# Kernel optimization log

Hardware: AMD Instinct MI355X
Metric: run time of the kernel (lower is better)

Reference implementation:

```python
import jax, jax.numpy as jnp
import numpy as np

N_SRC, N_MID, N_TGT = 200000, 100000, 50000
E1, E2 = 1600000, 800000
D_IN, D_HID, D_OUT = 128, 256, 64


def setup_inputs() -> dict:
    key = jax.random.key(0)
    ks = jax.random.split(key, 10)
    x = jax.random.normal(ks[0], (N_SRC, D_IN), dtype=jnp.float32)
    # edge_index[0] = source node ids, edge_index[1] = target node ids (PyG source_to_target)
    ei1 = jnp.stack([
        jax.random.randint(ks[1], (E1,), 0, N_SRC, dtype=jnp.int32),
        jax.random.randint(ks[2], (E1,), 0, N_MID, dtype=jnp.int32),
    ])
    ei2 = jnp.stack([
        jax.random.randint(ks[3], (E2,), 0, N_MID, dtype=jnp.int32),
        jax.random.randint(ks[4], (E2,), 0, N_TGT, dtype=jnp.int32),
    ])
    s = 1.0 / np.sqrt(D_IN)
    Wl1 = jax.random.uniform(ks[5], (D_IN, D_HID), jnp.float32, -s, s)
    Wr1 = jax.random.uniform(ks[6], (D_IN, D_HID), jnp.float32, -s, s)
    b1 = jnp.zeros((D_HID,), jnp.float32)
    s2 = 1.0 / np.sqrt(D_HID)
    Wl2 = jax.random.uniform(ks[7], (D_HID, D_OUT), jnp.float32, -s2, s2)
    Wr2 = jax.random.uniform(ks[8], (D_HID, D_OUT), jnp.float32, -s2, s2)
    b2 = jnp.zeros((D_OUT,), jnp.float32)
    return {"x": x, "edge_index1": ei1, "edge_index2": ei2,
            "Wl1": Wl1, "Wr1": Wr1, "b1": b1,
            "Wl2": Wl2, "Wr2": Wr2, "b2": b2}


def _sage_conv(x_src, x_tgt, edge_index, Wl, Wr, b, n_tgt):
    # mean aggregation of source features onto targets, then two linear branches
    msg = x_src[edge_index[0]]                                   # [E, d]
    agg = jax.ops.segment_sum(msg, edge_index[1], num_segments=n_tgt)
    cnt = jax.ops.segment_sum(jnp.ones((edge_index.shape[1],), x_src.dtype),
                              edge_index[1], num_segments=n_tgt)
    agg = agg / jnp.maximum(cnt, 1.0)[:, None]
    return agg @ Wl + x_tgt @ Wr + b


def reference(x, edge_index1, edge_index2, Wl1, Wr1, b1, Wl2, Wr2, b2):
    # layer 1: [N_SRC, D_IN] -> [N_MID, D_HID], then ReLU (dropout inactive in eval)
    h = _sage_conv(x, x[:N_MID], edge_index1, Wl1, Wr1, b1, N_MID)
    h = jax.nn.relu(h)
    # layer 2 (final): no activation
    out = _sage_conv(h, h[:N_TGT], edge_index2, Wl2, Wr2, b2, N_TGT)
    return out
```

## Files before the change

### kernel.cpp

```cpp
#include <hip/hip_runtime.h>


#define NSRC 200000
#define NMID 100000
#define NTGT 50000
#define NE1  1600000
#define NE2  800000
#define DIN  128
#define DHID 256
#define DOUT 64

#define XCH (NSRC * 16)

#define CH   4096
#define NBK1 391
#define NBK2 196
#define NCH1 ((NE1 + CH - 1) / CH)
#define NCH2 ((NE2 + CH - 1) / CH)
#define HCH  8192
#define NHC1 ((NE1 + HCH - 1) / HCH)
#define NHC2 ((NE2 + HCH - 1) / HCH)
#define NHIST (NHC1 + NHC2)
#define CVB ((XCH + 65536 + 32768 + 255) / 256)
#define MAXBUF 6144

typedef __attribute__((ext_vector_type(8))) short bf16x8;
typedef __attribute__((ext_vector_type(4))) float f32x4;
typedef __attribute__((ext_vector_type(2))) float f32x2;

__device__ __forceinline__ unsigned short f2bf(float f) {
    unsigned int u = __builtin_bit_cast(unsigned int, f);
    u += 0x7FFFu + ((u >> 16) & 1u);
    return (unsigned short)(u >> 16);
}
__device__ __forceinline__ float bf_lo(unsigned int u) {
    return __builtin_bit_cast(float, u << 16);
}
__device__ __forceinline__ float bf_hi(unsigned int u) {
    return __builtin_bit_cast(float, u & 0xFFFF0000u);
}
__device__ __forceinline__ float bf1(unsigned short u) {
    return __builtin_bit_cast(float, (unsigned int)u << 16);
}

__global__ __launch_bounds__(256) void conv_hist_kernel(
    const float* __restrict__ x,
    const float* __restrict__ Wl1, const float* __restrict__ Wr1,
    const float* __restrict__ Wl2, const float* __restrict__ Wr2,
    unsigned short* __restrict__ xb, unsigned short* __restrict__ WT1,
    unsigned short* __restrict__ WT2,
    const int* __restrict__ ei1, const int* __restrict__ ei2,
    int* __restrict__ bhist1, int* __restrict__ bhist2)
{
    __shared__ unsigned int lh[512];
    if (blockIdx.x < NHIST) {
        const int* ei; int* bh; int nE, nbk, chunk;
        if (blockIdx.x < NHC1) { ei = ei1; bh = bhist1; nE = NE1; nbk = NBK1; chunk = blockIdx.x; }
        else { ei = ei2; bh = bhist2; nE = NE2; nbk = NBK2; chunk = blockIdx.x - NHC1; }
        int t = threadIdx.x;
        lh[t] = 0; lh[t + 256] = 0;
        __syncthreads();
        int base = chunk * HCH;
        int end = nE < base + HCH ? nE : base + HCH;
        for (int e = base + t; e < end; e += 256)
            atomicAdd(&lh[((unsigned)ei[nE + e]) >> 8], 1u);
        __syncthreads();
        if (t < nbk && lh[t]) atomicAdd(&bh[t], (int)lh[t]);
        if (t + 256 < nbk && lh[t + 256]) atomicAdd(&bh[t + 256], (int)lh[t + 256]);
        return;
    }
    int gid = (blockIdx.x - NHIST) * 256 + threadIdx.x;
    if (gid < XCH) {
        const float4 v0 = *(const float4*)(x + (long long)gid * 8);
        const float4 v1 = *(const float4*)(x + (long long)gid * 8 + 4);
        unsigned short o[8] = {f2bf(v0.x), f2bf(v0.y), f2bf(v0.z), f2bf(v0.w),
                               f2bf(v1.x), f2bf(v1.y), f2bf(v1.z), f2bf(v1.w)};
        *(uint4*)(xb + (long long)gid * 8) = *(const uint4*)o;
        return;
    }
    int g = gid - XCH;
    if (g < 65536) {
        int n = g >> 8, k = g & 255;
        float v = (k < DIN) ? Wl1[(long long)k * DHID + n]
                            : Wr1[(long long)(k - DIN) * DHID + n];
        WT1[g] = f2bf(v);
        return;
    }
    g -= 65536;
    if (g < 32768) {
        int n2 = g >> 8, k = g & 255;
        float v = (n2 < DOUT) ? Wl2[(long long)k * DOUT + n2]
                              : Wr2[(long long)k * DOUT + (n2 - DOUT)];
        WT2[g] = f2bf(v);
    }
}


__global__ __launch_bounds__(256) void bucket_scan_kernel(
    const int* __restrict__ bhist1, const int* __restrict__ bhist2,
    int* __restrict__ bbase1, int* __restrict__ bbase2,
    int* __restrict__ bcur1, int* __restrict__ bcur2,
    int* __restrict__ rs1, int* __restrict__ rs2)
{
    __shared__ int s[256];
    int t = threadIdx.x;
    int a0 = (2 * t < NBK1) ? bhist1[2 * t] : 0;
    int a1 = (2 * t + 1 < NBK1) ? bhist1[2 * t + 1] : 0;
    s[t] = a0 + a1;
    __syncthreads();
    for (int off = 1; off < 256; off <<= 1) {
        int u = (t >= off) ? s[t - off] : 0;
        __syncthreads();
        s[t] += u;
        __syncthreads();
    }
    int ex = (t > 0) ? s[t - 1] : 0;
    if (2 * t < NBK1)     { bbase1[2 * t] = ex;      bcur1[2 * t] = ex; }
    if (2 * t + 1 < NBK1) { bbase1[2 * t + 1] = ex + a0; bcur1[2 * t + 1] = ex + a0; }
    if (t == 0) { bbase1[NBK1] = NE1; rs1[NMID] = NE1; bbase2[NBK2] = NE2; rs2[NTGT] = NE2; }
    __syncthreads();
    int b0 = (t < NBK2) ? bhist2[t] : 0;
    s[t] = b0;
    __syncthreads();
    for (int off = 1; off < 256; off <<= 1) {
        int u = (t >= off) ? s[t - off] : 0;
        __syncthreads();
        s[t] += u;
        __syncthreads();
    }
    int ex2 = (t > 0) ? s[t - 1] : 0;
    if (t < NBK2) { bbase2[t] = ex2; bcur2[t] = ex2; }
}

__global__ __launch_bounds__(256) void bin_kernel(
    const int* __restrict__ ei1, const int* __restrict__ ei2,
    int* __restrict__ bcur1, int* __restrict__ bcur2,
    uint2* __restrict__ gbuf1, uint2* __restrict__ gbuf2)
{
    __shared__ unsigned int lcnt[512];
    __shared__ unsigned int lofs[512];
    __shared__ unsigned int lpos[512];
    __shared__ unsigned int gbase[512];
    __shared__ unsigned int swarp[256];
    __shared__ uint2 lbuf[CH];

    const int* ei; int* bcur; uint2* gbuf; int nE, nbk, chunk;
    if (blockIdx.x < NCH1) {
        ei = ei1; bcur = bcur1; gbuf = gbuf1; nE = NE1; nbk = NBK1; chunk = blockIdx.x;
    } else {
        ei = ei2; bcur = bcur2; gbuf = gbuf2; nE = NE2; nbk = NBK2; chunk = blockIdx.x - NCH1;
    }
    int base = chunk * CH;
    int nb = nE - base; if (nb > CH) nb = CH;
    int t = threadIdx.x;

    for (int i = t; i < 512; i += 256) { lcnt[i] = 0; lpos[i] = 0; }
    __syncthreads();

    int srcv[16], tgtv[16];
    #pragma unroll
    for (int i = 0; i < 16; ++i) {
        int e = base + i * 256 + t;
        if (e < nE) {
            tgtv[i] = ei[nE + e];
            srcv[i] = ei[e];
            atomicAdd(&lcnt[tgtv[i] >> 8], 1u);
        } else tgtv[i] = -1;
    }
    __syncthreads();

    unsigned a0 = lcnt[2 * t], a1 = lcnt[2 * t + 1];
    swarp[t] = a0 + a1;
    __syncthreads();
    for (int off = 1; off < 256; off <<= 1) {
        unsigned v = (t >= off) ? swarp[t - off] : 0;
        __syncthreads();
        swarp[t] += v;
        __syncthreads();
    }
    unsigned ex = (t > 0) ? swarp[t - 1] : 0;
    lofs[2 * t] = ex;
    lofs[2 * t + 1] = ex + a0;
    if (2 * t < nbk && a0) gbase[2 * t] = atomicAdd(&bcur[2 * t], (int)a0);
    if (2 * t + 1 < nbk && a1) gbase[2 * t + 1] = atomicAdd(&bcur[2 * t + 1], (int)a1);
    __syncthreads();

    #pragma unroll
    for (int i = 0; i < 16; ++i) {
        if (tgtv[i] >= 0) {
            int b = tgtv[i] >> 8;
            unsigned idx = lofs[b] + atomicAdd(&lpos[b], 1u);
            lbuf[idx] = make_uint2((unsigned)srcv[i], (unsigned)tgtv[i]);
        }
    }
    __syncthreads();

    for (int i = t; i < nb; i += 256) {
        uint2 r = lbuf[i];
        int b = (int)(r.y >> 8);
        unsigned gi = gbase[b] + ((unsigned)i - lofs[b]);
        gbuf[gi] = r;
    }
}

__global__ __launch_bounds__(256) void bucket_csr_kernel(
    const uint2* __restrict__ gbuf1, const uint2* __restrict__ gbuf2,
    const int* __restrict__ bbase1, const int* __restrict__ bbase2,
    int* __restrict__ rs1, int* __restrict__ rs2,
    int* __restrict__ csr1, int* __restrict__ csr2)
{
    __shared__ unsigned int lhist[256];
    __shared__ unsigned int lcur[256];
    __shared__ unsigned int sscan[256];
    __shared__ unsigned int lbuf[MAXBUF];
    const uint2* gbuf; const int* bbase; int* rs; int* csr; int bucket, ntot;
    if (blockIdx.x < NBK1) {
        gbuf = gbuf1; bbase = bbase1; rs = rs1; csr = csr1; bucket = blockIdx.x; ntot = NMID;
    } else {
        gbuf = gbuf2; bbase = bbase2; rs = rs2; csr = csr2; bucket = blockIdx.x - NBK1; ntot = NTGT;
    }
    int base = bbase[bucket];
    int size = bbase[bucket + 1] - base;
    int node0 = bucket << 8;
    int nnode = ntot - node0; if (nnode > 256) nnode = 256;
    int t = threadIdx.x;
    lhist[t] = 0;
    __syncthreads();
    for (int i = t; i < size; i += 256)
        atomicAdd(&lhist[gbuf[base + i].y & 255], 1u);
    __syncthreads();
    unsigned v = lhist[t];
    sscan[t] = v;
    __syncthreads();
    for (int off = 1; off < 256; off <<= 1) {
        unsigned u = (t >= off) ? sscan[t - off] : 0;
        __syncthreads();
        sscan[t] += u;
        __syncthreads();
    }
    unsigned ex = (t > 0) ? sscan[t - 1] : 0;
    lcur[t] = ex;
    if (t < nnode) rs[node0 + t] = base + (int)ex;
    __syncthreads();
    for (int i = t; i < size; i += 256) {
        uint2 r = gbuf[base + i];
        unsigned pos = atomicAdd(&lcur[r.y & 255], 1u);
        lbuf[pos] = r.x;
    }
    __syncthreads();
    for (int i = t; i < size; i += 256)
        csr[base + i] = (int)lbuf[i];
}


__global__ __launch_bounds__(256) void gather1_kernel(
    const unsigned short* __restrict__ xb, const int* __restrict__ rs,
    const int* __restrict__ csr, unsigned short* __restrict__ aggnb)
{
    int wid = threadIdx.x >> 6;
    int lane = threadIdx.x & 63;
    int node = __builtin_amdgcn_readfirstlane(blockIdx.x * 4 + wid);
    if (node >= NMID) return;
    int s = rs[node];
    int d = rs[node + 1] - s;
    const unsigned int* xw = (const unsigned int*)xb;
    f32x2 a0 = {0.f, 0.f}, a1 = {0.f, 0.f}, a2 = {0.f, 0.f}, a3 = {0.f, 0.f};
    int j = 0;
    for (; j + 3 < d; j += 4) {
        int i0 = csr[s + j];
        int i1 = csr[s + j + 1];
        int i2 = csr[s + j + 2];
        int i3 = csr[s + j + 3];
        unsigned int u0 = xw[((size_t)(unsigned)i0 << 6) + lane];
        unsigned int u1 = xw[((size_t)(unsigned)i1 << 6) + lane];
        unsigned int u2 = xw[((size_t)(unsigned)i2 << 6) + lane];
        unsigned int u3 = xw[((size_t)(unsigned)i3 << 6) + lane];
        a0 += (f32x2){bf_lo(u0), bf_hi(u0)};
        a1 += (f32x2){bf_lo(u1), bf_hi(u1)};
        a2 += (f32x2){bf_lo(u2), bf_hi(u2)};
        a3 += (f32x2){bf_lo(u3), bf_hi(u3)};
    }
    for (; j < d; ++j) {
        int i0 = csr[s + j];
        unsigned int u0 = xw[((size_t)(unsigned)i0 << 6) + lane];
        a0 += (f32x2){bf_lo(u0), bf_hi(u0)};
    }
    float inv = (d > 0) ? 1.0f / (float)d : 0.f;
    f32x2 r = (a0 + a1) + (a2 + a3);
    float r0 = r.x * inv;
    float r1 = r.y * inv;
    unsigned int packed = (unsigned int)f2bf(r0) | ((unsigned int)f2bf(r1) << 16);
    *(unsigned int*)(aggnb + (long long)node * DIN + lane * 2) = packed;
}

__global__ __launch_bounds__(256) void gather2_final_kernel(
    const unsigned short* __restrict__ pb, const float* __restrict__ qb,
    const int* __restrict__ rs, const int* __restrict__ csr,
    float* __restrict__ out)
{
    int wid = threadIdx.x >> 6;
    int lane = threadIdx.x & 63;
    int node = __builtin_amdgcn_readfirstlane(blockIdx.x * 4 + wid);
    if (node >= NTGT) return;
    int s = rs[node];
    int d = rs[node + 1] - s;
    float a0 = 0.f, a1 = 0.f, a2 = 0.f, a3 = 0.f;
    int j = 0;
    for (; j + 3 < d; j += 4) {
        int i0 = csr[s + j];
        int i1 = csr[s + j + 1];
        int i2 = csr[s + j + 2];
        int i3 = csr[s + j + 3];
        a0 += bf1(pb[((size_t)(unsigned)i0 << 6) + lane]);
        a1 += bf1(pb[((size_t)(unsigned)i1 << 6) + lane]);
        a2 += bf1(pb[((size_t)(unsigned)i2 << 6) + lane]);
        a3 += bf1(pb[((size_t)(unsigned)i3 << 6) + lane]);
    }
    for (; j < d; ++j) {
        int i0 = csr[s + j];
        a0 += bf1(pb[((size_t)(unsigned)i0 << 6) + lane]);
    }
    float inv = (d > 0) ? 1.0f / (float)d : 0.f;
    out[(long long)node * DOUT + lane] =
        qb[(long long)node * DOUT + lane] + ((a0 + a1) + (a2 + a3)) * inv;
}

#define LDSP 40

__global__ __launch_bounds__(256) void gemm1_mfma(
    const unsigned short* __restrict__ aggnb, const unsigned short* __restrict__ xb,
    const unsigned short* __restrict__ WT, const float* __restrict__ bias,
    unsigned short* __restrict__ h)
{
    __shared__ unsigned short Asm[128 * LDSP];
    __shared__ unsigned short Bsm[128 * LDSP];
    const int tid = threadIdx.x;
    const int bm = blockIdx.x * 128;
    const int bn = blockIdx.y * 128;
    const int wave = tid >> 6, lane = tid & 63;
    const int wr = wave >> 1, wc = wave & 1;
    const int lrow = lane & 15, quad = lane >> 4;

    const int c0r = tid >> 2, c0s = tid & 3;
    const int c1r = (tid + 256) >> 2, c1s = tid & 3;
    int growA0 = bm + c0r; if (growA0 >= NMID) growA0 = NMID - 1;
    int growA1 = bm + c1r; if (growA1 >= NMID) growA1 = NMID - 1;

    uint4 pa0, pa1, pb0, pb1;
    auto gload = [&](int k0) {
        int gk0 = k0 + c0s * 8;
        const unsigned short* sA0 = (gk0 < DIN)
            ? (aggnb + (long long)growA0 * DIN + gk0)
            : (xb + (long long)growA0 * DIN + (gk0 - DIN));
        pa0 = *(const uint4*)sA0;
        const unsigned short* sA1 = (gk0 < DIN)
            ? (aggnb + (long long)growA1 * DIN + gk0)
            : (xb + (long long)growA1 * DIN + (gk0 - DIN));
        pa1 = *(const uint4*)sA1;
        pb0 = *(const uint4*)(WT + (long long)(bn + c0r) * 256 + k0 + c0s * 8);
        pb1 = *(const uint4*)(WT + (long long)(bn + c1r) * 256 + k0 + c1s * 8);
    };

    f32x4 acc[4][4];
    #pragma unroll
    for (int i = 0; i < 4; ++i)
        #pragma unroll
        for (int j = 0; j < 4; ++j)
            acc[i][j] = (f32x4){0.f, 0.f, 0.f, 0.f};

    gload(0);
    for (int it = 0; it < 8; ++it) {
        if (it) __syncthreads();
        *(uint4*)(Asm + c0r * LDSP + c0s * 8) = pa0;
        *(uint4*)(Asm + c1r * LDSP + c1s * 8) = pa1;
        *(uint4*)(Bsm + c0r * LDSP + c0s * 8) = pb0;
        *(uint4*)(Bsm + c1r * LDSP + c1s * 8) = pb1;
        __syncthreads();
        if (it < 7) gload((it + 1) * 32);
        bf16x8 af[4], bfr[4];
        #pragma unroll
        for (int mi = 0; mi < 4; ++mi)
            af[mi] = *(const bf16x8*)(Asm + (wr * 64 + mi * 16 + lrow) * LDSP + quad * 8);
        #pragma unroll
        for (int ni = 0; ni < 4; ++ni)
            bfr[ni] = *(const bf16x8*)(Bsm + (wc * 64 + ni * 16 + lrow) * LDSP + quad * 8);
        #pragma unroll
        for (int mi = 0; mi < 4; ++mi)
            #pragma unroll
            for (int ni = 0; ni < 4; ++ni)
                acc[mi][ni] = __builtin_amdgcn_mfma_f32_16x16x32_bf16(
                    af[mi], bfr[ni], acc[mi][ni], 0, 0, 0);
    }
    #pragma unroll
    for (int mi = 0; mi < 4; ++mi) {
        #pragma unroll
        for (int ni = 0; ni < 4; ++ni) {
            int col = bn + wc * 64 + ni * 16 + lrow;
            float bv = bias[col];
            #pragma unroll
            for (int r = 0; r < 4; ++r) {
                int row = bm + wr * 64 + mi * 16 + quad * 4 + r;
                if (row < NMID) {
                    float v = acc[mi][ni][r] + bv;
                    h[(long long)row * DHID + col] = f2bf(fmaxf(v, 0.0f));
                }
            }
        }
    }
}

__global__ __launch_bounds__(256) void gemm2_dual_mfma(
    const unsigned short* __restrict__ h, const unsigned short* __restrict__ WT2,
    const float* __restrict__ b2,
    unsigned short* __restrict__ pb, float* __restrict__ qb)
{
    __shared__ unsigned short Asm[128 * LDSP];
    __shared__ unsigned short Bsm[128 * LDSP];
    const int tid = threadIdx.x;
    const int bm = blockIdx.x * 128;
    const int wave = tid >> 6, lane = tid & 63;
    const int lrow = lane & 15, quad = lane >> 4;
    const bool doq = (bm < NTGT);

    const int c0r = tid >> 2, c0s = tid & 3;
    const int c1r = (tid + 256) >> 2;
    int growA0 = bm + c0r; if (growA0 >= NMID) growA0 = NMID - 1;
    int growA1 = bm + c1r; if (growA1 >= NMID) growA1 = NMID - 1;

    uint4 pa0, pa1, pb0, pb1;
    auto gload = [&](int k0) {
        pa0 = *(const uint4*)(h + (long long)growA0 * DHID + k0 + c0s * 8);
        pa1 = *(const uint4*)(h + (long long)growA1 * DHID + k0 + c0s * 8);
        pb0 = *(const uint4*)(WT2 + (long long)c0r * 256 + k0 + c0s * 8);
        pb1 = *(const uint4*)(WT2 + (long long)c1r * 256 + k0 + c0s * 8);
    };

    f32x4 accP[2][4], accQ[2][4];
    #pragma unroll
    for (int i = 0; i < 2; ++i)
        #pragma unroll
        for (int j = 0; j < 4; ++j) {
            accP[i][j] = (f32x4){0.f, 0.f, 0.f, 0.f};
            accQ[i][j] = (f32x4){0.f, 0.f, 0.f, 0.f};
        }

    gload(0);
    for (int it = 0; it < 8; ++it) {
        if (it) __syncthreads();
        *(uint4*)(Asm + c0r * LDSP + c0s * 8) = pa0;
        *(uint4*)(Asm + c1r * LDSP + c0s * 8) = pa1;
        *(uint4*)(Bsm + c0r * LDSP + c0s * 8) = pb0;
        *(uint4*)(Bsm + c1r * LDSP + c0s * 8) = pb1;
        __syncthreads();
        if (it < 7) gload((it + 1) * 32);
        bf16x8 af[2], bp[4];
        #pragma unroll
        for (int mi = 0; mi < 2; ++mi)
            af[mi] = *(const bf16x8*)(Asm + (wave * 32 + mi * 16 + lrow) * LDSP + quad * 8);
        #pragma unroll
        for (int ni = 0; ni < 4; ++ni)
            bp[ni] = *(const bf16x8*)(Bsm + (ni * 16 + lrow) * LDSP + quad * 8);
        #pragma unroll
        for (int mi = 0; mi < 2; ++mi)
            #pragma unroll
            for (int ni = 0; ni < 4; ++ni)
                accP[mi][ni] = __builtin_amdgcn_mfma_f32_16x16x32_bf16(
                    af[mi], bp[ni], accP[mi][ni], 0, 0, 0);
        if (doq) {
            bf16x8 bq[4];
            #pragma unroll
            for (int ni = 0; ni < 4; ++ni)
                bq[ni] = *(const bf16x8*)(Bsm + (64 + ni * 16 + lrow) * LDSP + quad * 8);
            #pragma unroll
            for (int mi = 0; mi < 2; ++mi)
                #pragma unroll
                for (int ni = 0; ni < 4; ++ni)
                    accQ[mi][ni] = __builtin_amdgcn_mfma_f32_16x16x32_bf16(
                        af[mi], bq[ni], accQ[mi][ni], 0, 0, 0);
        }
    }
    #pragma unroll
    for (int mi = 0; mi < 2; ++mi) {
        #pragma unroll
        for (int ni = 0; ni < 4; ++ni) {
            int col = ni * 16 + lrow;
            #pragma unroll
            for (int r = 0; r < 4; ++r) {
                int row = bm + wave * 32 + mi * 16 + quad * 4 + r;
                if (row < NMID)
                    pb[(long long)row * DOUT + col] = f2bf(accP[mi][ni][r]);
                if (doq && row < NTGT)
                    qb[(long long)row * DOUT + col] = accQ[mi][ni][r] + b2[col];
            }
        }
    }
}

extern "C" void kernel_launch(void* const* d_in, const int* in_sizes, int n_in,
                              void* d_out, int out_size, void* d_ws, size_t ws_size,
                              hipStream_t stream) {
    const float* x   = (const float*)d_in[0];
    const int*   ei1 = (const int*)d_in[1];
    const int*   ei2 = (const int*)d_in[2];
    const float* Wl1 = (const float*)d_in[3];
    const float* Wr1 = (const float*)d_in[4];
    const float* b1  = (const float*)d_in[5];
    const float* Wl2 = (const float*)d_in[6];
    const float* Wr2 = (const float*)d_in[7];
    const float* b2  = (const float*)d_in[8];
    float* out = (float*)d_out;

    unsigned short* xb    = (unsigned short*)d_ws;
    unsigned short* aggnb = xb + (size_t)NSRC * DIN;
    unsigned short* h     = aggnb + (size_t)NMID * DIN;
    unsigned short* WT1   = h + (size_t)NMID * DHID;
    unsigned short* WT2   = WT1 + 256 * 256;
    unsigned short* pb    = WT2 + 128 * 256;
    float* qb   = (float*)(pb + (size_t)NMID * DOUT);
    int* rs1    = (int*)(qb + (size_t)NTGT * DOUT);
    int* rs2    = rs1 + (NMID + 1);
    int* bhist1 = rs2 + (NTGT + 1);
    int* bhist2 = bhist1 + NBK1;
    int* bbase1 = bhist2 + NBK2;
    int* bbase2 = bbase1 + (NBK1 + 1);
    int* bcur1  = bbase2 + (NBK2 + 1);
    int* bcur2  = bcur1 + NBK1;
    int* csr1   = bcur2 + NBK2 + 1;
    int* csr2   = csr1 + NE1;
    uint2* gbuf1 = (uint2*)(((size_t)(csr2 + NE2) + 15) & ~(size_t)15);
    uint2* gbuf2 = gbuf1 + NE1;

    hipMemsetAsync(bhist1, 0, (size_t)(NBK1 + NBK2) * 4, stream);
    conv_hist_kernel<<<NHIST + CVB, 256, 0, stream>>>(
        x, Wl1, Wr1, Wl2, Wr2, xb, WT1, WT2, ei1, ei2, bhist1, bhist2);
    bucket_scan_kernel<<<1, 256, 0, stream>>>(bhist1, bhist2, bbase1, bbase2,
                                              bcur1, bcur2, rs1, rs2);
    bin_kernel<<<NCH1 + NCH2, 256, 0, stream>>>(ei1, ei2, bcur1, bcur2, gbuf1, gbuf2);
    bucket_csr_kernel<<<NBK1 + NBK2, 256, 0, stream>>>(
        gbuf1, gbuf2, bbase1, bbase2, rs1, rs2, csr1, csr2);

    gather1_kernel<<<(NMID + 3) / 4, 256, 0, stream>>>(xb, rs1, csr1, aggnb);
    {
        dim3 grid((NMID + 127) / 128, 2);
        gemm1_mfma<<<grid, 256, 0, stream>>>(aggnb, xb, WT1, b1, h);
    }
    gemm2_dual_mfma<<<(NMID + 127) / 128, 256, 0, stream>>>(h, WT2, b2, pb, qb);
    gather2_final_kernel<<<(NTGT + 3) / 4, 256, 0, stream>>>(pb, qb, rs2, csr2, out);
}
```

Before: 388.7 us.

## Stage full A tile once in gemm1 and gather two neighbors per wave in gather2

gemm1 now loads the whole 128x256 concatenated A tile (agg and x) into LDS once and loops over both 128-column output halves inside one block. This removes the second grid row that re-read A from global memory. The cost is much more LDS per block, which may lower occupancy. gather2_final has each half-wave fetch a different neighbor row as 32-bit packed bf16 pairs, then combines the halves with a cross-lane shuffle, raising the number of independent loads in flight.

```diff
diff --git a/kernel.cpp b/kernel.cpp
--- a/kernel.cpp
+++ b/kernel.cpp
@@ -300,109 +300,139 @@
 {
     int wid = threadIdx.x >> 6;
     int lane = threadIdx.x & 63;
+    int hh = lane >> 5;
+    int c  = lane & 31;
     int node = __builtin_amdgcn_readfirstlane(blockIdx.x * 4 + wid);
     if (node >= NTGT) return;
     int s = rs[node];
     int d = rs[node + 1] - s;
-    float a0 = 0.f, a1 = 0.f, a2 = 0.f, a3 = 0.f;
+    const unsigned int* pw = (const unsigned int*)pb;
+    f32x2 a0 = {0.f, 0.f}, a1 = {0.f, 0.f}, a2 = {0.f, 0.f}, a3 = {0.f, 0.f};
     int j = 0;
-    for (; j + 3 < d; j += 4) {
-        int i0 = csr[s + j];
-        int i1 = csr[s + j + 1];
-        int i2 = csr[s + j + 2];
-        int i3 = csr[s + j + 3];
-        a0 += bf1(pb[((size_t)(unsigned)i0 << 6) + lane]);
-        a1 += bf1(pb[((size_t)(unsigned)i1 << 6) + lane]);
-        a2 += bf1(pb[((size_t)(unsigned)i2 << 6) + lane]);
-        a3 += bf1(pb[((size_t)(unsigned)i3 << 6) + lane]);
-    }
-    for (; j < d; ++j) {
-        int i0 = csr[s + j];
-        a0 += bf1(pb[((size_t)(unsigned)i0 << 6) + lane]);
-    }
-    float inv = (d > 0) ? 1.0f / (float)d : 0.f;
-    out[(long long)node * DOUT + lane] =
-        qb[(long long)node * DOUT + lane] + ((a0 + a1) + (a2 + a3)) * inv;
+    for (; j + 8 <= d; j += 8) {
+        int e0 = csr[s + j + 0], e1 = csr[s + j + 1];
+        int e2 = csr[s + j + 2], e3 = csr[s + j + 3];
+        int e4 = csr[s + j + 4], e5 = csr[s + j + 5];
+        int e6 = csr[s + j + 6], e7 = csr[s + j + 7];
+        int i0 = hh ? e1 : e0;
+        int i1 = hh ? e3 : e2;
+        int i2 = hh ? e5 : e4;
+        int i3 = hh ? e7 : e6;
+        unsigned u0 = pw[((size_t)(unsigned)i0 << 5) + c];
+        unsigned u1 = pw[((size_t)(unsigned)i1 << 5) + c];
+        unsigned u2 = pw[((size_t)(unsigned)i2 << 5) + c];
+        unsigned u3 = pw[((size_t)(unsigned)i3 << 5) + c];
+        a0 += (f32x2){bf_lo(u0), bf_hi(u0)};
+        a1 += (f32x2){bf_lo(u1), bf_hi(u1)};
+        a2 += (f32x2){bf_lo(u2), bf_hi(u2)};
+        a3 += (f32x2){bf_lo(u3), bf_hi(u3)};
+    }
+    for (; j < d; j += 2) {
+        int rem = d - j;
+        int ea = csr[s + j];
+        int eb = (rem > 1) ? csr[s + j + 1] : ea;
+        if (hh < rem) {
+            int ia = hh ? eb : ea;
+            unsigned ua = pw[((size_t)(unsigned)ia << 5) + c];
+            a0 += (f32x2){bf_lo(ua), bf_hi(ua)};
+        }
+    }
+    f32x2 t = (a0 + a1) + (a2 + a3);
+    t.x += __shfl_xor(t.x, 32);
+    t.y += __shfl_xor(t.y, 32);
+    if (hh == 0) {
+        float inv = (d > 0) ? 1.0f / (float)d : 0.f;
+        const float2 qv = *(const float2*)(qb + (long long)node * DOUT + c * 2);
+        float2 o;
+        o.x = qv.x + t.x * inv;
+        o.y = qv.y + t.y * inv;
+        *(float2*)(out + (long long)node * DOUT + c * 2) = o;
+    }
 }
 
 #define LDSP 40
+#define LDSK 264
 
 __global__ __launch_bounds__(256) void gemm1_mfma(
     const unsigned short* __restrict__ aggnb, const unsigned short* __restrict__ xb,
     const unsigned short* __restrict__ WT, const float* __restrict__ bias,
     unsigned short* __restrict__ h)
 {
-    __shared__ unsigned short Asm[128 * LDSP];
+    __shared__ unsigned short Asm[128 * LDSK];
     __shared__ unsigned short Bsm[128 * LDSP];
     const int tid = threadIdx.x;
     const int bm = blockIdx.x * 128;
-    const int bn = blockIdx.y * 128;
     const int wave = tid >> 6, lane = tid & 63;
     const int wr = wave >> 1, wc = wave & 1;
     const int lrow = lane & 15, quad = lane >> 4;
 
     const int c0r = tid >> 2, c0s = tid & 3;
-    const int c1r = (tid + 256) >> 2, c1s = tid & 3;
-    int growA0 = bm + c0r; if (growA0 >= NMID) growA0 = NMID - 1;
-    int growA1 = bm + c1r; if (growA1 >= NMID) growA1 = NMID - 1;
-
-    uint4 pa0, pa1, pb0, pb1;
-    auto gload = [&](int k0) {
-        int gk0 = k0 + c0s * 8;
-        const unsigned short* sA0 = (gk0 < DIN)
-            ? (aggnb + (long long)growA0 * DIN + gk0)
-            : (xb + (long long)growA0 * DIN + (gk0 - DIN));
-        pa0 = *(const uint4*)sA0;
-        const unsigned short* sA1 = (gk0 < DIN)
-            ? (aggnb + (long long)growA1 * DIN + gk0)
-            : (xb + (long long)growA1 * DIN + (gk0 - DIN));
-        pa1 = *(const uint4*)sA1;
-        pb0 = *(const uint4*)(WT + (long long)(bn + c0r) * 256 + k0 + c0s * 8);
-        pb1 = *(const uint4*)(WT + (long long)(bn + c1r) * 256 + k0 + c1s * 8);
+    const int c1r = c0r + 64;
+
+    uint4 pb0, pb1;
+    auto gloadB = [&](int st) {
+        int bnS = st >> 3, itS = st & 7;
+        int k0 = itS * 32;
+        pb0 = *(const uint4*)(WT + (long long)(bnS * 128 + c0r) * 256 + k0 + c0s * 8);
+        pb1 = *(const uint4*)(WT + (long long)(bnS * 128 + c1r) * 256 + k0 + c0s * 8);
     };
+    gloadB(0);
+
+    #pragma unroll
+    for (int cc = 0; cc < 16; ++cc) {
+        int seg = cc * 256 + tid;
+        int row = seg >> 5;
+        int ks  = (seg & 31) * 8;
+        int grow = bm + row; if (grow >= NMID) grow = NMID - 1;
+        const unsigned short* src = (ks < DIN)
+            ? (aggnb + (long long)grow * DIN + ks)
+            : (xb + (long long)grow * DIN + (ks - DIN));
+        *(uint4*)(Asm + row * LDSK + ks) = *(const uint4*)src;
+    }
 
     f32x4 acc[4][4];
-    #pragma unroll
-    for (int i = 0; i < 4; ++i)
-        #pragma unroll
-        for (int j = 0; j < 4; ++j)
-            acc[i][j] = (f32x4){0.f, 0.f, 0.f, 0.f};
-
-    gload(0);
-    for (int it = 0; it < 8; ++it) {
-        if (it) __syncthreads();
-        *(uint4*)(Asm + c0r * LDSP + c0s * 8) = pa0;
-        *(uint4*)(Asm + c1r * LDSP + c1s * 8) = pa1;
-        *(uint4*)(Bsm + c0r * LDSP + c0s * 8) = pb0;
-        *(uint4*)(Bsm + c1r * LDSP + c1s * 8) = pb1;
-        __syncthreads();
-        if (it < 7) gload((it + 1) * 32);
-        bf16x8 af[4], bfr[4];
-        #pragma unroll
-        for (int mi = 0; mi < 4; ++mi)
-            af[mi] = *(const bf16x8*)(Asm + (wr * 64 + mi * 16 + lrow) * LDSP + quad * 8);
-        #pragma unroll
-        for (int ni = 0; ni < 4; ++ni)
-            bfr[ni] = *(const bf16x8*)(Bsm + (wc * 64 + ni * 16 + lrow) * LDSP + quad * 8);
-        #pragma unroll
-        for (int mi = 0; mi < 4; ++mi)
+    for (int bn = 0; bn < 2; ++bn) {
+        #pragma unroll
+        for (int i = 0; i < 4; ++i)
+            #pragma unroll
+            for (int j = 0; j < 4; ++j)
+                acc[i][j] = (f32x4){0.f, 0.f, 0.f, 0.f};
+        for (int it = 0; it < 8; ++it) {
+            __syncthreads();
+            *(uint4*)(Bsm + c0r * LDSP + c0s * 8) = pb0;
+            *(uint4*)(Bsm + c1r * LDSP + c0s * 8) = pb1;
+            __syncthreads();
+            int st = bn * 8 + it;
+            if (st < 15) gloadB(st + 1);
+            bf16x8 af[4], bfr[4];
+            #pragma unroll
+            for (int mi = 0; mi < 4; ++mi)
+                af[mi] = *(const bf16x8*)(Asm + (wr * 64 + mi * 16 + lrow) * LDSK
+                                          + it * 32 + quad * 8);
             #pragma unroll
             for (int ni = 0; ni < 4; ++ni)
-                acc[mi][ni] = __builtin_amdgcn_mfma_f32_16x16x32_bf16(
-                    af[mi], bfr[ni], acc[mi][ni], 0, 0, 0);
-    }
-    #pragma unroll
-    for (int mi = 0; mi < 4; ++mi) {
-        #pragma unroll
-        for (int ni = 0; ni < 4; ++ni) {
-            int col = bn + wc * 64 + ni * 16 + lrow;
-            float bv = bias[col];
-            #pragma unroll
-            for (int r = 0; r < 4; ++r) {
-                int row = bm + wr * 64 + mi * 16 + quad * 4 + r;
-                if (row < NMID) {
-                    float v = acc[mi][ni][r] + bv;
-                    h[(long long)row * DHID + col] = f2bf(fmaxf(v, 0.0f));
+                bfr[ni] = *(const bf16x8*)(Bsm + (wc * 64 + ni * 16 + lrow) * LDSP
+                                           + quad * 8);
+            #pragma unroll
+            for (int mi = 0; mi < 4; ++mi)
+                #pragma unroll
+                for (int ni = 0; ni < 4; ++ni)
+                    acc[mi][ni] = __builtin_amdgcn_mfma_f32_16x16x32_bf16(
+                        af[mi], bfr[ni], acc[mi][ni], 0, 0, 0);
+        }
+        #pragma unroll
+        for (int mi = 0; mi < 4; ++mi) {
+            #pragma unroll
+            for (int ni = 0; ni < 4; ++ni) {
+                int col = bn * 128 + wc * 64 + ni * 16 + lrow;
+                float bv = bias[col];
+                #pragma unroll
+                for (int r = 0; r < 4; ++r) {
+                    int row = bm + wr * 64 + mi * 16 + quad * 4 + r;
+                    if (row < NMID) {
+                        float v = acc[mi][ni][r] + bv;
+                        h[(long long)row * DHID + col] = f2bf(fmaxf(v, 0.0f));
+                    }
                 }
             }
         }
@@ -540,10 +570,7 @@
         gbuf1, gbuf2, bbase1, bbase2, rs1, rs2, csr1, csr2);
 
     gather1_kernel<<<(NMID + 3) / 4, 256, 0, stream>>>(xb, rs1, csr1, aggnb);
-    {
-        dim3 grid((NMID + 127) / 128, 2);
-        gemm1_mfma<<<grid, 256, 0, stream>>>(aggnb, xb, WT1, b1, h);
-    }
+    gemm1_mfma<<<(NMID + 127) / 128, 256, 0, stream>>>(aggnb, xb, WT1, b1, h);
     gemm2_dual_mfma<<<(NMID + 127) / 128, 256, 0, stream>>>(h, WT2, b2, pb, qb);
     gather2_final_kernel<<<(NTGT + 3) / 4, 256, 0, stream>>>(pb, qb, rs2, csr2, out);
 }
```

After: 393.0 us. No clear change (+1.1%).

## Fold bucket scan into histogram kernel, overlap CSR2 build with gather1, widen gather2

Applied to the files above, without the earlier changes.

The last histogram block, detected through an atomic done-counter, now performs the bucket prefix scan, which removes the separate single-block scan launch. The CSR build is split so layer 2's CSR construction runs in the same launch as the layer-1 gather, overlapping independent work and dropping a kernel boundary. The final gather reads packed bf16 pairs and splits each wave into two halves that handle alternate edges, then combines them with a shuffle. The done-counter relies on a threadfence plus atomic reads being enough for cross-block visibility, and the fused CSR2 blocks need large LDS, which may lower occupancy for the gather blocks.

```diff
diff --git a/kernel.cpp b/kernel.cpp
--- a/kernel.cpp
+++ b/kernel.cpp
@@ -23,6 +23,7 @@
 #define NHIST (NHC1 + NHC2)
 #define CVB ((XCH + 65536 + 32768 + 255) / 256)
 #define MAXBUF 6144
+#define G1BLK ((NMID + 3) / 4)
 
 typedef __attribute__((ext_vector_type(8))) short bf16x8;
 typedef __attribute__((ext_vector_type(4))) float f32x4;
@@ -38,9 +39,6 @@
 }
 __device__ __forceinline__ float bf_hi(unsigned int u) {
     return __builtin_bit_cast(float, u & 0xFFFF0000u);
-}
-__device__ __forceinline__ float bf1(unsigned short u) {
-    return __builtin_bit_cast(float, (unsigned int)u << 16);
 }
 
 __global__ __launch_bounds__(256) void conv_hist_kernel(
@@ -50,14 +48,19 @@
     unsigned short* __restrict__ xb, unsigned short* __restrict__ WT1,
     unsigned short* __restrict__ WT2,
     const int* __restrict__ ei1, const int* __restrict__ ei2,
-    int* __restrict__ bhist1, int* __restrict__ bhist2)
+    int* __restrict__ bhist1, int* __restrict__ bhist2,
+    int* __restrict__ donecnt,
+    int* __restrict__ bbase1, int* __restrict__ bbase2,
+    int* __restrict__ bcur1, int* __restrict__ bcur2,
+    int* __restrict__ rs1, int* __restrict__ rs2)
 {
     __shared__ unsigned int lh[512];
+    __shared__ int sdone;
+    int t = threadIdx.x;
     if (blockIdx.x < NHIST) {
         const int* ei; int* bh; int nE, nbk, chunk;
         if (blockIdx.x < NHC1) { ei = ei1; bh = bhist1; nE = NE1; nbk = NBK1; chunk = blockIdx.x; }
         else { ei = ei2; bh = bhist2; nE = NE2; nbk = NBK2; chunk = blockIdx.x - NHC1; }
-        int t = threadIdx.x;
         lh[t] = 0; lh[t + 256] = 0;
         __syncthreads();
         int base = chunk * HCH;
@@ -67,9 +70,40 @@
         __syncthreads();
         if (t < nbk && lh[t]) atomicAdd(&bh[t], (int)lh[t]);
         if (t + 256 < nbk && lh[t + 256]) atomicAdd(&bh[t + 256], (int)lh[t + 256]);
+        __threadfence();
+        if (t == 0) sdone = atomicAdd(donecnt, 1);
+        __syncthreads();
+        if (sdone != NHIST - 1) return;
+        int* s = (int*)lh;
+        int a0 = (2 * t < NBK1) ? atomicAdd(&bhist1[2 * t], 0) : 0;
+        int a1 = (2 * t + 1 < NBK1) ? atomicAdd(&bhist1[2 * t + 1], 0) : 0;
+        s[t] = a0 + a1;
+        __syncthreads();
+        for (int off = 1; off < 256; off <<= 1) {
+            int u = (t >= off) ? s[t - off] : 0;
+            __syncthreads();
+            s[t] += u;
+            __syncthreads();
+        }
+        int ex = (t > 0) ? s[t - 1] : 0;
+        if (2 * t < NBK1)     { bbase1[2 * t] = ex;          bcur1[2 * t] = ex; }
+        if (2 * t + 1 < NBK1) { bbase1[2 * t + 1] = ex + a0; bcur1[2 * t + 1] = ex + a0; }
+        if (t == 0) { bbase1[NBK1] = NE1; rs1[NMID] = NE1; bbase2[NBK2] = NE2; rs2[NTGT] = NE2; }
+        __syncthreads();
+        int b0 = (t < NBK2) ? atomicAdd(&bhist2[t], 0) : 0;
+        s[t] = b0;
+        __syncthreads();
+        for (int off = 1; off < 256; off <<= 1) {
+            int u = (t >= off) ? s[t - off] : 0;
+            __syncthreads();
+            s[t] += u;
+            __syncthreads();
+        }
+        int ex2 = (t > 0) ? s[t - 1] : 0;
+        if (t < NBK2) { bbase2[t] = ex2; bcur2[t] = ex2; }
         return;
     }
-    int gid = (blockIdx.x - NHIST) * 256 + threadIdx.x;
+    int gid = (blockIdx.x - NHIST) * 256 + t;
     if (gid < XCH) {
         const float4 v0 = *(const float4*)(x + (long long)gid * 8);
         const float4 v1 = *(const float4*)(x + (long long)gid * 8 + 4);
@@ -93,43 +127,6 @@
                               : Wr2[(long long)k * DOUT + (n2 - DOUT)];
         WT2[g] = f2bf(v);
     }
-}
-
-
-__global__ __launch_bounds__(256) void bucket_scan_kernel(
-    const int* __restrict__ bhist1, const int* __restrict__ bhist2,
-    int* __restrict__ bbase1, int* __restrict__ bbase2,
-    int* __restrict__ bcur1, int* __restrict__ bcur2,
-    int* __restrict__ rs1, int* __restrict__ rs2)
-{
-    __shared__ int s[256];
-    int t = threadIdx.x;
-    int a0 = (2 * t < NBK1) ? bhist1[2 * t] : 0;
-    int a1 = (2 * t + 1 < NBK1) ? bhist1[2 * t + 1] : 0;
-    s[t] = a0 + a1;
-    __syncthreads();
-    for (int off = 1; off < 256; off <<= 1) {
-        int u = (t >= off) ? s[t - off] : 0;
-        __syncthreads();
-        s[t] += u;
-        __syncthreads();
-    }
-    int ex = (t > 0) ? s[t - 1] : 0;
-    if (2 * t < NBK1)     { bbase1[2 * t] = ex;      bcur1[2 * t] = ex; }
-    if (2 * t + 1 < NBK1) { bbase1[2 * t + 1] = ex + a0; bcur1[2 * t + 1] = ex + a0; }
-    if (t == 0) { bbase1[NBK1] = NE1; rs1[NMID] = NE1; bbase2[NBK2] = NE2; rs2[NTGT] = NE2; }
-    __syncthreads();
-    int b0 = (t < NBK2) ? bhist2[t] : 0;
-    s[t] = b0;
-    __syncthreads();
-    for (int off = 1; off < 256; off <<= 1) {
-        int u = (t >= off) ? s[t - off] : 0;
-        __syncthreads();
-        s[t] += u;
-        __syncthreads();
-    }
-    int ex2 = (t > 0) ? s[t - 1] : 0;
-    if (t < NBK2) { bbase2[t] = ex2; bcur2[t] = ex2; }
 }
 
 __global__ __launch_bounds__(256) void bin_kernel(
@@ -203,26 +200,19 @@
     }
 }
 
-__global__ __launch_bounds__(256) void bucket_csr_kernel(
-    const uint2* __restrict__ gbuf1, const uint2* __restrict__ gbuf2,
-    const int* __restrict__ bbase1, const int* __restrict__ bbase2,
-    int* __restrict__ rs1, int* __restrict__ rs2,
-    int* __restrict__ csr1, int* __restrict__ csr2)
+__global__ __launch_bounds__(256) void csr1_kernel(
+    const uint2* __restrict__ gbuf, const int* __restrict__ bbase,
+    int* __restrict__ rs, int* __restrict__ csr)
 {
     __shared__ unsigned int lhist[256];
     __shared__ unsigned int lcur[256];
     __shared__ unsigned int sscan[256];
     __shared__ unsigned int lbuf[MAXBUF];
-    const uint2* gbuf; const int* bbase; int* rs; int* csr; int bucket, ntot;
-    if (blockIdx.x < NBK1) {
-        gbuf = gbuf1; bbase = bbase1; rs = rs1; csr = csr1; bucket = blockIdx.x; ntot = NMID;
-    } else {
-        gbuf = gbuf2; bbase = bbase2; rs = rs2; csr = csr2; bucket = blockIdx.x - NBK1; ntot = NTGT;
-    }
+    int bucket = blockIdx.x;
     int base = bbase[bucket];
     int size = bbase[bucket + 1] - base;
     int node0 = bucket << 8;
-    int nnode = ntot - node0; if (nnode > 256) nnode = 256;
+    int nnode = NMID - node0; if (nnode > 256) nnode = 256;
     int t = threadIdx.x;
     lhist[t] = 0;
     __syncthreads();
@@ -252,25 +242,65 @@
         csr[base + i] = (int)lbuf[i];
 }
 
-
-__global__ __launch_bounds__(256) void gather1_kernel(
-    const unsigned short* __restrict__ xb, const int* __restrict__ rs,
-    const int* __restrict__ csr, unsigned short* __restrict__ aggnb)
+__global__ __launch_bounds__(256) void csr2_gather1_kernel(
+    const uint2* __restrict__ gbuf2, const int* __restrict__ bbase2,
+    int* __restrict__ rs2, int* __restrict__ csr2,
+    const unsigned short* __restrict__ xb, const int* __restrict__ rs1,
+    const int* __restrict__ csr1, unsigned short* __restrict__ aggnb)
 {
-    int wid = threadIdx.x >> 6;
-    int lane = threadIdx.x & 63;
-    int node = __builtin_amdgcn_readfirstlane(blockIdx.x * 4 + wid);
+    __shared__ unsigned int lhist[256];
+    __shared__ unsigned int lcur[256];
+    __shared__ unsigned int sscan[256];
+    __shared__ unsigned int lbuf[MAXBUF];
+    int t = threadIdx.x;
+    if (blockIdx.x < NBK2) {
+        int bucket = blockIdx.x;
+        int base = bbase2[bucket];
+        int size = bbase2[bucket + 1] - base;
+        int node0 = bucket << 8;
+        int nnode = NTGT - node0; if (nnode > 256) nnode = 256;
+        lhist[t] = 0;
+        __syncthreads();
+        for (int i = t; i < size; i += 256)
+            atomicAdd(&lhist[gbuf2[base + i].y & 255], 1u);
+        __syncthreads();
+        unsigned v = lhist[t];
+        sscan[t] = v;
+        __syncthreads();
+        for (int off = 1; off < 256; off <<= 1) {
+            unsigned u = (t >= off) ? sscan[t - off] : 0;
+            __syncthreads();
+            sscan[t] += u;
+            __syncthreads();
+        }
+        unsigned ex = (t > 0) ? sscan[t - 1] : 0;
+        lcur[t] = ex;
+        if (t < nnode) rs2[node0 + t] = base + (int)ex;
+        __syncthreads();
+        for (int i = t; i < size; i += 256) {
+            uint2 r = gbuf2[base + i];
+            unsigned pos = atomicAdd(&lcur[r.y & 255], 1u);
+            lbuf[pos] = r.x;
+        }
+        __syncthreads();
+        for (int i = t; i < size; i += 256)
+            csr2[base + i] = (int)lbuf[i];
+        return;
+    }
+    int wid = t >> 6;
+    int lane = t & 63;
+    int node = __builtin_amdgcn_readfirstlane((blockIdx.x - NBK2) * 4 + wid);
     if (node >= NMID) return;
-    int s = rs[node];
-    int d = rs[node + 1] - s;
+    int s = rs1[node];
+    int d = rs1[node + 1] - s;
     const unsigned int* xw = (const unsigned int*)xb;
     f32x2 a0 = {0.f, 0.f}, a1 = {0.f, 0.f}, a2 = {0.f, 0.f}, a3 = {0.f, 0.f};
     int j = 0;
     for (; j + 3 < d; j += 4) {
-        int i0 = csr[s + j];
-        int i1 = csr[s + j + 1];
-        int i2 = csr[s + j + 2];
-        int i3 = csr[s + j + 3];
+        int i0 = csr1[s + j];
+        int i1 = csr1[s + j + 1];
+        int i2 = csr1[s + j + 2];
+        int i3 = csr1[s + j + 3];
         unsigned int u0 = xw[((size_t)(unsigned)i0 << 6) + lane];
         unsigned int u1 = xw[((size_t)(unsigned)i1 << 6) + lane];
         unsigned int u2 = xw[((size_t)(unsigned)i2 << 6) + lane];
@@ -281,15 +311,14 @@
         a3 += (f32x2){bf_lo(u3), bf_hi(u3)};
     }
     for (; j < d; ++j) {
-        int i0 = csr[s + j];
+        int i0 = csr1[s + j];
         unsigned int u0 = xw[((size_t)(unsigned)i0 << 6) + lane];
         a0 += (f32x2){bf_lo(u0), bf_hi(u0)};
     }
     float inv = (d > 0) ? 1.0f / (float)d : 0.f;
     f32x2 r = (a0 + a1) + (a2 + a3);
-    float r0 = r.x * inv;
-    float r1 = r.y * inv;
-    unsigned int packed = (unsigned int)f2bf(r0) | ((unsigned int)f2bf(r1) << 16);
+    unsigned int packed =
+        (unsigned int)f2bf(r.x * inv) | ((unsigned int)f2bf(r.y * inv) << 16);
     *(unsigned int*)(aggnb + (long long)node * DIN + lane * 2) = packed;
 }
 
@@ -300,29 +329,54 @@
 {
     int wid = threadIdx.x >> 6;
     int lane = threadIdx.x & 63;
+    int hh = lane >> 5;
+    int c  = lane & 31;
     int node = __builtin_amdgcn_readfirstlane(blockIdx.x * 4 + wid);
     if (node >= NTGT) return;
     int s = rs[node];
     int d = rs[node + 1] - s;
-    float a0 = 0.f, a1 = 0.f, a2 = 0.f, a3 = 0.f;
+    const unsigned int* pw = (const unsigned int*)pb;
+    f32x2 a0 = {0.f, 0.f}, a1 = {0.f, 0.f}, a2 = {0.f, 0.f}, a3 = {0.f, 0.f};
     int j = 0;
-    for (; j + 3 < d; j += 4) {
-        int i0 = csr[s + j];
-        int i1 = csr[s + j + 1];
-        int i2 = csr[s + j + 2];
-        int i3 = csr[s + j + 3];
-        a0 += bf1(pb[((size_t)(unsigned)i0 << 6) + lane]);
-        a1 += bf1(pb[((size_t)(unsigned)i1 << 6) + lane]);
-        a2 += bf1(pb[((size_t)(unsigned)i2 << 6) + lane]);
-        a3 += bf1(pb[((size_t)(unsigned)i3 << 6) + lane]);
-    }
-    for (; j < d; ++j) {
-        int i0 = csr[s + j];
-        a0 += bf1(pb[((size_t)(unsigned)i0 << 6) + lane]);
-    }
-    float inv = (d > 0) ? 1.0f / (float)d : 0.f;
-    out[(long long)node * DOUT + lane] =
-        qb[(long long)node * DOUT + lane] + ((a0 + a1) + (a2 + a3)) * inv;
+    for (; j + 8 <= d; j += 8) {
+        int e0 = csr[s + j + 0], e1 = csr[s + j + 1];
+        int e2 = csr[s + j + 2], e3 = csr[s + j + 3];
+        int e4 = csr[s + j + 4], e5 = csr[s + j + 5];
+        int e6 = csr[s + j + 6], e7 = csr[s + j + 7];
+        int i0 = hh ? e1 : e0;
+        int i1 = hh ? e3 : e2;
+        int i2 = hh ? e5 : e4;
+        int i3 = hh ? e7 : e6;
+        unsigned u0 = pw[((size_t)(unsigned)i0 << 5) + c];
+        unsigned u1 = pw[((size_t)(unsigned)i1 << 5) + c];
+        unsigned u2 = pw[((size_t)(unsigned)i2 << 5) + c];
+        unsigned u3 = pw[((size_t)(unsigned)i3 << 5) + c];
+        a0 += (f32x2){bf_lo(u0), bf_hi(u0)};
+        a1 += (f32x2){bf_lo(u1), bf_hi(u1)};
+        a2 += (f32x2){bf_lo(u2), bf_hi(u2)};
+        a3 += (f32x2){bf_lo(u3), bf_hi(u3)};
+    }
+    for (; j < d; j += 2) {
+        int rem = d - j;
+        int ea = csr[s + j];
+        int eb = (rem > 1) ? csr[s + j + 1] : ea;
+        if (hh < rem) {
+            int ia = hh ? eb : ea;
+            unsigned ua = pw[((size_t)(unsigned)ia << 5) + c];
+            a0 += (f32x2){bf_lo(ua), bf_hi(ua)};
+        }
+    }
+    f32x2 tt = (a0 + a1) + (a2 + a3);
+    tt.x += __shfl_xor(tt.x, 32);
+    tt.y += __shfl_xor(tt.y, 32);
+    if (hh == 0) {
+        float inv = (d > 0) ? 1.0f / (float)d : 0.f;
+        const float2 qv = *(const float2*)(qb + (long long)node * DOUT + c * 2);
+        float2 o;
+        o.x = qv.x + tt.x * inv;
+        o.y = qv.y + tt.y * inv;
+        *(float2*)(out + (long long)node * DOUT + c * 2) = o;
+    }
 }
 
 #define LDSP 40
@@ -516,30 +570,29 @@
     unsigned short* WT1   = h + (size_t)NMID * DHID;
     unsigned short* WT2   = WT1 + 256 * 256;
     unsigned short* pb    = WT2 + 128 * 256;
-    float* qb   = (float*)(pb + (size_t)NMID * DOUT);
-    int* rs1    = (int*)(qb + (size_t)NTGT * DOUT);
-    int* rs2    = rs1 + (NMID + 1);
-    int* bhist1 = rs2 + (NTGT + 1);
-    int* bhist2 = bhist1 + NBK1;
-    int* bbase1 = bhist2 + NBK2;
-    int* bbase2 = bbase1 + (NBK1 + 1);
-    int* bcur1  = bbase2 + (NBK2 + 1);
-    int* bcur2  = bcur1 + NBK1;
-    int* csr1   = bcur2 + NBK2 + 1;
-    int* csr2   = csr1 + NE1;
+    float* qb    = (float*)(pb + (size_t)NMID * DOUT);
+    int* rs1     = (int*)(qb + (size_t)NTGT * DOUT);
+    int* rs2     = rs1 + (NMID + 1);
+    int* bhist1  = rs2 + (NTGT + 1);
+    int* bhist2  = bhist1 + NBK1;
+    int* donecnt = bhist2 + NBK2;
+    int* bbase1  = donecnt + 1;
+    int* bbase2  = bbase1 + (NBK1 + 1);
+    int* bcur1   = bbase2 + (NBK2 + 1);
+    int* bcur2   = bcur1 + NBK1;
+    int* csr1    = bcur2 + NBK2 + 1;
+    int* csr2    = csr1 + NE1;
     uint2* gbuf1 = (uint2*)(((size_t)(csr2 + NE2) + 15) & ~(size_t)15);
     uint2* gbuf2 = gbuf1 + NE1;
 
-    hipMemsetAsync(bhist1, 0, (size_t)(NBK1 + NBK2) * 4, stream);
+    hipMemsetAsync(bhist1, 0, (size_t)(NBK1 + NBK2 + 1) * 4, stream);
     conv_hist_kernel<<<NHIST + CVB, 256, 0, stream>>>(
-        x, Wl1, Wr1, Wl2, Wr2, xb, WT1, WT2, ei1, ei2, bhist1, bhist2);
-    bucket_scan_kernel<<<1, 256, 0, stream>>>(bhist1, bhist2, bbase1, bbase2,
-                                              bcur1, bcur2, rs1, rs2);
+        x, Wl1, Wr1, Wl2, Wr2, xb, WT1, WT2, ei1, ei2, bhist1, bhist2,
+        donecnt, bbase1, bbase2, bcur1, bcur2, rs1, rs2);
     bin_kernel<<<NCH1 + NCH2, 256, 0, stream>>>(ei1, ei2, bcur1, bcur2, gbuf1, gbuf2);
-    bucket_csr_kernel<<<NBK1 + NBK2, 256, 0, stream>>>(
-        gbuf1, gbuf2, bbase1, bbase2, rs1, rs2, csr1, csr2);
-
-    gather1_kernel<<<(NMID + 3) / 4, 256, 0, stream>>>(xb, rs1, csr1, aggnb);
+    csr1_kernel<<<NBK1, 256, 0, stream>>>(gbuf1, bbase1, rs1, csr1);
+    csr2_gather1_kernel<<<NBK2 + G1BLK, 256, 0, stream>>>(
+        gbuf2, bbase2, rs2, csr2, xb, rs1, csr1, aggnb);
     {
         dim3 grid((NMID + 127) / 128, 2);
         gemm1_mfma<<<grid, 256, 0, stream>>>(aggnb, xb, WT1, b1, h);
```

Result: slower. 418.9 us (+7.8%).
